# Performance work log

Measured on AMD Instinct MI355X. Metric: run time of the kernel, lower is better.

Reference implementation:

```python
import jax, jax.numpy as jnp
import numpy as np

N_NODES = 20000
N_EDGES = 640000
F_IN = 128
HID = 128


def setup_inputs() -> dict:
    key = jax.random.key(0)
    ks = jax.random.split(key, 12)
    d = {}
    d["x"] = jax.random.normal(ks[0], (N_NODES, F_IN), dtype=jnp.float32)
    d["edge_index"] = jax.random.randint(ks[1], (2, N_EDGES), 0, N_NODES, dtype=jnp.int64)
    d["edge_weight"] = jax.random.uniform(ks[2], (N_EDGES,), dtype=jnp.float32)
    d["h"] = jax.random.normal(ks[3], (N_NODES, HID), dtype=jnp.float32)
    s1 = 1.0 / np.sqrt(F_IN)
    s2 = 1.0 / np.sqrt(HID)
    s3 = 1.0 / np.sqrt(2 * HID)
    d["W1"] = jax.random.uniform(ks[4], (F_IN, HID), jnp.float32, -s1, s1)
    d["b1"] = jnp.zeros((HID,), jnp.float32)
    d["W2"] = jax.random.uniform(ks[5], (HID, HID), jnp.float32, -s2, s2)
    d["b2"] = jnp.zeros((HID,), jnp.float32)
    d["Wu"] = jax.random.uniform(ks[6], (2 * HID, HID), jnp.float32, -s3, s3)
    d["bu"] = jax.random.uniform(ks[7], (HID,), jnp.float32, -s3, s3)
    d["Wr"] = jax.random.uniform(ks[8], (2 * HID, HID), jnp.float32, -s3, s3)
    d["br"] = jax.random.uniform(ks[9], (HID,), jnp.float32, -s3, s3)
    d["Wc"] = jax.random.uniform(ks[10], (2 * HID, HID), jnp.float32, -s3, s3)
    d["bc"] = jax.random.uniform(ks[11], (HID,), jnp.float32, -s3, s3)
    return d


def _gcn_layer(x, W, b, src, dst, norm, n):
    # GCNConv: transform then normalized scatter-add aggregation
    xw = x @ W                                    # [N, out]
    agg = jax.ops.segment_sum(xw[src] * norm[:, None], dst, num_segments=n)
    return agg + b


def reference(x, edge_index, edge_weight, h, W1, b1, W2, b2, Wu, bu, Wr, br, Wc, bc):
    n = x.shape[0]
    loops = jnp.arange(n, dtype=edge_index.dtype)
    src = jnp.concatenate([edge_index[0], loops])
    dst = jnp.concatenate([edge_index[1], loops])
    ew = jnp.concatenate([edge_weight, jnp.ones((n,), edge_weight.dtype)])
    # symmetric GCN normalization with self-loops
    deg = jax.ops.segment_sum(ew, dst, num_segments=n)
    dinv = jnp.where(deg > 0, jax.lax.rsqrt(deg), 0.0)
    norm = dinv[src] * ew * dinv[dst]             # [E+N]
    # 2-layer GCN: in->hid (ReLU) -> hid->hid
    h1 = jax.nn.relu(_gcn_layer(x, W1, b1, src, dst, norm, n))
    g = _gcn_layer(h1, W2, b2, src, dst, norm, n)
    xg = jax.nn.sigmoid(g)                        # [N, HID]
    # GRU-style gating
    xh = jnp.concatenate([xg, h], axis=-1)        # [N, 2*HID]
    u = jax.nn.sigmoid(xh @ Wu + bu)
    r = jax.nn.sigmoid(xh @ Wr + br)
    c = jnp.tanh(jnp.concatenate([xg, r * h], axis=-1) @ Wc + bc)
    return u * h + (1.0 - u) * c
```

## Files before the change

### kernel.cpp

```cpp
#include <hip/hip_runtime.h>
#include <math.h>

#define N_NODES 20000
#define N_EDGES 640000
#define HID 128
#define NPAD 20224
#define NBLK 79

typedef __attribute__((ext_vector_type(8))) short bf16x8;
typedef __attribute__((ext_vector_type(4))) float f32x4;

#define FIX_SCALE 274877906944.0
#define FIX_MASK ((1ull << 48) - 1)

__device__ inline short f2bf(float f) {
    unsigned u = __builtin_bit_cast(unsigned, f);
    u += 0x7fffu + ((u >> 16) & 1u);
    return (short)(u >> 16);
}
__device__ inline float bf2f(short s) {
    unsigned u = ((unsigned)(unsigned short)s) << 16;
    return __builtin_bit_cast(float, u);
}
__device__ inline float4 unpack_bf4(uint2 v) {
    float4 f;
    f.x = __builtin_bit_cast(float, v.x << 16);
    f.y = __builtin_bit_cast(float, v.x & 0xffff0000u);
    f.z = __builtin_bit_cast(float, v.y << 16);
    f.w = __builtin_bit_cast(float, v.y & 0xffff0000u);
    return f;
}
__device__ inline uint2 pack_bf4(float4 f) {
    uint2 v;
    v.x = (unsigned)(unsigned short)f2bf(f.x) | ((unsigned)(unsigned short)f2bf(f.y) << 16);
    v.y = (unsigned)(unsigned short)f2bf(f.z) | ((unsigned)(unsigned short)f2bf(f.w) << 16);
    return v;
}

__global__ __launch_bounds__(256) void k_init(unsigned long long* packed) {
    int i = blockIdx.x * 256 + threadIdx.x;
    if (i < 4 * NPAD) packed[i] = 0ull;
}

__global__ __launch_bounds__(256) void k_hist(unsigned long long* packed, int* __restrict__ rank,
                                              const int* __restrict__ dst,
                                              const float* __restrict__ ew) {
    int e = blockIdx.x * 256 + threadIdx.x;
    int shard = blockIdx.x & 3;
    if (e < N_EDGES) {
        int d = dst[e];
        unsigned long long add = (1ull << 48) | (unsigned long long)((double)ew[e] * FIX_SCALE);
        unsigned long long old = atomicAdd(&packed[shard * NPAD + d], add);
        rank[e] = (int)(old >> 48);
    }
}

__global__ __launch_bounds__(256) void k_scan_part(const unsigned long long* __restrict__ packed,
                                                   int* __restrict__ tot, int* __restrict__ bsum) {
    __shared__ int red[256];
    int tid = threadIdx.x;
    int i = blockIdx.x * 256 + tid;
    int t = 0;
    if (i < N_NODES) {
#pragma unroll
        for (int s = 0; s < 4; s++) t += (int)(packed[s * NPAD + i] >> 48);
        tot[i] = t;
    }
    red[tid] = t;
    __syncthreads();
    for (int off = 128; off > 0; off >>= 1) {
        if (tid < off) red[tid] += red[tid + off];
        __syncthreads();
    }
    if (tid == 0) bsum[blockIdx.x] = red[0];
}

__global__ __launch_bounds__(128) void k_scan_bsum(const int* __restrict__ bsum,
                                                   int* __restrict__ boff) {
    __shared__ int smem[128];
    int tid = threadIdx.x;
    int v = (tid < NBLK) ? bsum[tid] : 0;
    smem[tid] = v;
    __syncthreads();
    for (int off = 1; off < 128; off <<= 1) {
        int t = (tid >= off) ? smem[tid - off] : 0;
        __syncthreads();
        smem[tid] += t;
        __syncthreads();
    }
    if (tid < NBLK) boff[tid] = smem[tid] - v;
}

__global__ __launch_bounds__(256) void k_scan_final(const unsigned long long* __restrict__ packed,
                                                    const int* __restrict__ tot,
                                                    const int* __restrict__ boff,
                                                    int* __restrict__ rp, int* __restrict__ sb,
                                                    float* __restrict__ dinv) {
    __shared__ int smem[256];
    int tid = threadIdx.x;
    int i = blockIdx.x * 256 + tid;
    int t = (i < N_NODES) ? tot[i] : 0;
    smem[tid] = t;
    __syncthreads();
    for (int off = 1; off < 256; off <<= 1) {
        int x = (tid >= off) ? smem[tid - off] : 0;
        __syncthreads();
        smem[tid] += x;
        __syncthreads();
    }
    if (i < N_NODES) {
        int excl = smem[tid] - t + boff[blockIdx.x];
        rp[i] = excl;
        if (i == N_NODES - 1) rp[N_NODES] = excl + t;
        int acc = excl;
        double deg = 1.0;
#pragma unroll
        for (int s = 0; s < 4; s++) {
            unsigned long long p = packed[s * NPAD + i];
            sb[s * NPAD + i] = acc;
            acc += (int)(p >> 48);
            deg += (double)(p & FIX_MASK) * (1.0 / FIX_SCALE);
        }
        dinv[i] = rsqrtf((float)deg);
    }
}

__global__ __launch_bounds__(256) void k_fill(const int* __restrict__ src,
                                              const int* __restrict__ dst,
                                              const float* __restrict__ ew,
                                              const float* __restrict__ dinv,
                                              const int* __restrict__ sb,
                                              const int* __restrict__ rank,
                                              int2* __restrict__ csr) {
    int e = blockIdx.x * 256 + threadIdx.x;
    int shard = blockIdx.x & 3;
    if (e < N_EDGES) {
        int s = src[e], d = dst[e];
        int slot = sb[shard * NPAD + d] + rank[e];
        float w = dinv[s] * ew[e] * dinv[d];
        csr[slot] = make_int2(s, __builtin_bit_cast(int, w));
    }
}

__global__ __launch_bounds__(256) void k_cvt2(const float* __restrict__ x, const float* __restrict__ h,
                                              short* __restrict__ xb, short* __restrict__ hb) {
    const int NH4 = (N_NODES * HID) / 4;
    int i = blockIdx.x * 256 + threadIdx.x;
    const float* s; short* d; int idx;
    if (i < NH4) { s = x; d = xb; idx = i; } else { s = h; d = hb; idx = i - NH4; }
    float4 v = ((const float4*)s)[idx];
    short4 o;
    o.x = f2bf(v.x); o.y = f2bf(v.y); o.z = f2bf(v.z); o.w = f2bf(v.w);
    ((short4*)d)[idx] = o;
}

__global__ __launch_bounds__(256) void k_wcvt(const float* __restrict__ W1, const float* __restrict__ W2,
                                              const float* __restrict__ Wu, const float* __restrict__ Wr,
                                              const float* __restrict__ Wc,
                                              short* WT1, short* WT2, short* WTu, short* WTr, short* WTc) {
    int i = blockIdx.x * 256 + threadIdx.x;
    if (i < 32768) {
        const float* W = (i < 16384) ? W1 : W2;
        short* T = (i < 16384) ? WT1 : WT2;
        int j = i & 16383;
        int n = j >> 7, k = j & 127;
        T[n * 128 + k] = f2bf(W[k * 128 + n]);
    } else {
        int j = i - 32768;
        const float* W = Wu; short* T = WTu;
        if (j >= 65536)      { W = Wc; T = WTc; j -= 65536; }
        else if (j >= 32768) { W = Wr; T = WTr; j -= 32768; }
        int n = j >> 8, k = j & 255;
        T[n * 256 + k] = f2bf(W[k * 128 + n]);
    }
}

__global__ __launch_bounds__(256) void k_gemm_mfma(const short* __restrict__ Ab,
                                                   const short* __restrict__ WT,
                                                   short* __restrict__ Cb) {
    __shared__ short As[16 * 136];
    int tid = threadIdx.x;
    int r0 = blockIdx.x * 16;
    {
        int row = tid >> 4;
        int col0 = (tid & 15) * 8;
        *(bf16x8*)(&As[row * 136 + col0]) = *(const bf16x8*)(Ab + (size_t)(r0 + row) * HID + col0);
    }
    __syncthreads();
    int wave = tid >> 6, lane = tid & 63;
    int m = lane & 15, quad = lane >> 4;
    f32x4 acc[2];
    acc[0] = (f32x4){0.f, 0.f, 0.f, 0.f};
    acc[1] = acc[0];
#pragma unroll
    for (int ks = 0; ks < 4; ks++) {
        int k0 = ks * 32 + quad * 8;
        bf16x8 a = *(const bf16x8*)(&As[m * 136 + k0]);
#pragma unroll
        for (int j = 0; j < 2; j++) {
            int n = (wave * 2 + j) * 16 + m;
            bf16x8 b = *(const bf16x8*)(WT + n * 128 + k0);
            acc[j] = __builtin_amdgcn_mfma_f32_16x16x32_bf16(a, b, acc[j], 0, 0, 0);
        }
    }
#pragma unroll
    for (int j = 0; j < 2; j++) {
        int col = (wave * 2 + j) * 16 + m;
#pragma unroll
        for (int rg = 0; rg < 4; rg++) {
            int grow = r0 + quad * 4 + rg;
            Cb[(size_t)grow * HID + col] = f2bf(acc[j][rg]);
        }
    }
}

__global__ __launch_bounds__(256) void k_aggregate(const short* __restrict__ xw,
                                                   short* __restrict__ outb,
                                                   const int* __restrict__ rp,
                                                   const int2* __restrict__ csr,
                                                   const float* __restrict__ dinv,
                                                   const float* __restrict__ bias,
                                                   int act) {
    int node = blockIdx.x * 4 + (threadIdx.x >> 6);
    int lane = threadIdx.x & 63;
    int half = lane >> 5;
    int l = lane & 31;
    float4 acc = {0.f, 0.f, 0.f, 0.f};
    if (half == 0) {
        float dv = dinv[node];
        float dv2 = dv * dv;
        float4 v = unpack_bf4(((const uint2*)(xw + (size_t)node * HID))[l]);
        acc.x = v.x * dv2; acc.y = v.y * dv2; acc.z = v.z * dv2; acc.w = v.w * dv2;
    }
    int j = rp[node], end = rp[node + 1];
    for (; j + 7 < end; j += 8) {
        int2 e0 = csr[j + 0 + half];
        int2 e1 = csr[j + 2 + half];
        int2 e2 = csr[j + 4 + half];
        int2 e3 = csr[j + 6 + half];
        float4 v0 = unpack_bf4(((const uint2*)(xw + (size_t)e0.x * HID))[l]);
        float4 v1 = unpack_bf4(((const uint2*)(xw + (size_t)e1.x * HID))[l]);
        float4 v2 = unpack_bf4(((const uint2*)(xw + (size_t)e2.x * HID))[l]);
        float4 v3 = unpack_bf4(((const uint2*)(xw + (size_t)e3.x * HID))[l]);
        float w0 = __builtin_bit_cast(float, e0.y);
        float w1 = __builtin_bit_cast(float, e1.y);
        float w2 = __builtin_bit_cast(float, e2.y);
        float w3 = __builtin_bit_cast(float, e3.y);
        acc.x += v0.x * w0; acc.y += v0.y * w0; acc.z += v0.z * w0; acc.w += v0.w * w0;
        acc.x += v1.x * w1; acc.y += v1.y * w1; acc.z += v1.z * w1; acc.w += v1.w * w1;
        acc.x += v2.x * w2; acc.y += v2.y * w2; acc.z += v2.z * w2; acc.w += v2.w * w2;
        acc.x += v3.x * w3; acc.y += v3.y * w3; acc.z += v3.z * w3; acc.w += v3.w * w3;
    }
    for (; j + 1 < end; j += 2) {
        int2 e0 = csr[j + half];
        float4 v0 = unpack_bf4(((const uint2*)(xw + (size_t)e0.x * HID))[l]);
        float w0 = __builtin_bit_cast(float, e0.y);
        acc.x += v0.x * w0; acc.y += v0.y * w0; acc.z += v0.z * w0; acc.w += v0.w * w0;
    }
    if (j < end && half == 0) {
        int2 e0 = csr[j];
        float4 v0 = unpack_bf4(((const uint2*)(xw + (size_t)e0.x * HID))[l]);
        float w0 = __builtin_bit_cast(float, e0.y);
        acc.x += v0.x * w0; acc.y += v0.y * w0; acc.z += v0.z * w0; acc.w += v0.w * w0;
    }
    acc.x += __shfl_xor(acc.x, 32);
    acc.y += __shfl_xor(acc.y, 32);
    acc.z += __shfl_xor(acc.z, 32);
    acc.w += __shfl_xor(acc.w, 32);
    if (half == 0) {
        float4 b = ((const float4*)bias)[l];
        acc.x += b.x; acc.y += b.y; acc.z += b.z; acc.w += b.w;
        if (act == 0) {
            acc.x = fmaxf(acc.x, 0.f); acc.y = fmaxf(acc.y, 0.f);
            acc.z = fmaxf(acc.z, 0.f); acc.w = fmaxf(acc.w, 0.f);
        } else {
            acc.x = 1.f / (1.f + __expf(-acc.x)); acc.y = 1.f / (1.f + __expf(-acc.y));
            acc.z = 1.f / (1.f + __expf(-acc.z)); acc.w = 1.f / (1.f + __expf(-acc.w));
        }
        ((uint2*)(outb + (size_t)node * HID))[l] = pack_bf4(acc);
    }
}

__global__ __launch_bounds__(256) void k_gate(const short* __restrict__ xgb, const short* __restrict__ hb,
                                              const float* __restrict__ hf,
                                              const short* __restrict__ WTu, const short* __restrict__ WTr,
                                              const short* __restrict__ WTc,
                                              const float* __restrict__ pbu, const float* __restrict__ pbr,
                                              const float* __restrict__ pbc,
                                              float* __restrict__ out) {
    __shared__ short Xs[16 * 264];
    int tid = threadIdx.x;
    int r0 = blockIdx.x * 16;
#pragma unroll
    for (int i = 0; i < 2; i++) {
        int c = tid + i * 256;
        int row = c >> 5;
        int col0 = (c & 31) * 8;
        int grow = r0 + row;
        bf16x8 v;
        if (col0 < 128) v = *(const bf16x8*)(xgb + (size_t)grow * HID + col0);
        else            v = *(const bf16x8*)(hb + (size_t)grow * HID + (col0 - 128));
        *(bf16x8*)(&Xs[row * 264 + col0]) = v;
    }
    __syncthreads();
    int wave = tid >> 6, lane = tid & 63;
    int m = lane & 15, quad = lane >> 4;
    f32x4 au[2], ar[2];
    au[0] = (f32x4){0.f, 0.f, 0.f, 0.f};
    au[1] = au[0]; ar[0] = au[0]; ar[1] = au[0];
#pragma unroll
    for (int ks = 0; ks < 8; ks++) {
        int k0 = ks * 32 + quad * 8;
        bf16x8 a = *(const bf16x8*)(&Xs[m * 264 + k0]);
#pragma unroll
        for (int j = 0; j < 2; j++) {
            int n = (wave * 2 + j) * 16 + m;
            bf16x8 bu_f = *(const bf16x8*)(WTu + n * 256 + k0);
            au[j] = __builtin_amdgcn_mfma_f32_16x16x32_bf16(a, bu_f, au[j], 0, 0, 0);
            bf16x8 br_f = *(const bf16x8*)(WTr + n * 256 + k0);
            ar[j] = __builtin_amdgcn_mfma_f32_16x16x32_bf16(a, br_f, ar[j], 0, 0, 0);
        }
    }
    __syncthreads();
#pragma unroll
    for (int j = 0; j < 2; j++) {
        int col = (wave * 2 + j) * 16 + m;
        float brv = pbr[col];
#pragma unroll
        for (int rg = 0; rg < 4; rg++) {
            int trow = quad * 4 + rg;
            float rv = 1.f / (1.f + __expf(-(ar[j][rg] + brv)));
            float hv = bf2f(Xs[trow * 264 + 128 + col]);
            Xs[trow * 264 + 128 + col] = f2bf(rv * hv);
        }
    }
    __syncthreads();
    f32x4 ac[2];
    ac[0] = (f32x4){0.f, 0.f, 0.f, 0.f};
    ac[1] = ac[0];
#pragma unroll
    for (int ks = 0; ks < 8; ks++) {
        int k0 = ks * 32 + quad * 8;
        bf16x8 a = *(const bf16x8*)(&Xs[m * 264 + k0]);
#pragma unroll
        for (int j = 0; j < 2; j++) {
            int n = (wave * 2 + j) * 16 + m;
            bf16x8 bc_f = *(const bf16x8*)(WTc + n * 256 + k0);
            ac[j] = __builtin_amdgcn_mfma_f32_16x16x32_bf16(a, bc_f, ac[j], 0, 0, 0);
        }
    }
#pragma unroll
    for (int j = 0; j < 2; j++) {
        int col = (wave * 2 + j) * 16 + m;
        float buv = pbu[col], bcv = pbc[col];
#pragma unroll
        for (int rg = 0; rg < 4; rg++) {
            int grow = r0 + quad * 4 + rg;
            float uv = 1.f / (1.f + __expf(-(au[j][rg] + buv)));
            float cv = tanhf(ac[j][rg] + bcv);
            float hv = hf[(size_t)grow * HID + col];
            out[(size_t)grow * HID + col] = uv * hv + (1.f - uv) * cv;
        }
    }
}

extern "C" void kernel_launch(void* const* d_in, const int* in_sizes, int n_in,
                              void* d_out, int out_size, void* d_ws, size_t ws_size,
                              hipStream_t stream) {
    const float* x  = (const float*)d_in[0];
    const int*   ei = (const int*)d_in[1];
    const float* ew = (const float*)d_in[2];
    const float* h  = (const float*)d_in[3];
    const float* W1 = (const float*)d_in[4];
    const float* b1 = (const float*)d_in[5];
    const float* W2 = (const float*)d_in[6];
    const float* b2 = (const float*)d_in[7];
    const float* Wu = (const float*)d_in[8];
    const float* bu = (const float*)d_in[9];
    const float* Wr = (const float*)d_in[10];
    const float* br = (const float*)d_in[11];
    const float* Wc = (const float*)d_in[12];
    const float* bc = (const float*)d_in[13];
    const int* src = ei;
    const int* dst = ei + N_EDGES;
    float* out = (float*)d_out;

    const size_t NH = (size_t)N_NODES * HID;
    float* ws = (float*)d_ws;
    float* dinv = ws;
    int*   rp   = (int*)(ws + NPAD);
    unsigned long long* packed = (unsigned long long*)(ws + 2 * NPAD);
    int*   sb   = (int*)(ws + 10 * NPAD);
    int*   tot  = (int*)(ws + 14 * NPAD);
    int*   bsum = (int*)(ws + 15 * NPAD);
    int*   boff = (int*)(ws + 15 * NPAD + 128);
    int*   rank = (int*)(ws + 15 * NPAD + 256);
    int2*  csr  = (int2*)(ws + 15 * NPAD + 256 + N_EDGES);
    short* xb  = (short*)(ws + 15 * NPAD + 256 + 3 * N_EDGES);
    short* hb  = xb + NH;
    short* xw  = hb + NH;
    short* h1b = xw + NH;
    short* xgb = h1b + NH;
    short* WT1 = xgb + NH;
    short* WT2 = WT1 + 16384;
    short* WTu = WT2 + 16384;
    short* WTr = WTu + 32768;
    short* WTc = WTr + 32768;

    k_init<<<(4 * NPAD + 255) / 256, 256, 0, stream>>>(packed);
    k_hist<<<N_EDGES / 256, 256, 0, stream>>>(packed, rank, dst, ew);
    k_scan_part<<<NBLK, 256, 0, stream>>>(packed, tot, bsum);
    k_scan_bsum<<<1, 128, 0, stream>>>(bsum, boff);
    k_scan_final<<<NBLK, 256, 0, stream>>>(packed, tot, boff, rp, sb, dinv);
    k_fill<<<N_EDGES / 256, 256, 0, stream>>>(src, dst, ew, dinv, sb, rank, csr);

    k_cvt2<<<(int)(2 * NH / 1024), 256, 0, stream>>>(x, h, xb, hb);
    k_wcvt<<<512, 256, 0, stream>>>(W1, W2, Wu, Wr, Wc, WT1, WT2, WTu, WTr, WTc);

    k_gemm_mfma<<<N_NODES / 16, 256, 0, stream>>>(xb, WT1, xw);
    k_aggregate<<<N_NODES / 4, 256, 0, stream>>>(xw, h1b, rp, csr, dinv, b1, 0);
    k_gemm_mfma<<<N_NODES / 16, 256, 0, stream>>>(h1b, WT2, xw);
    k_aggregate<<<N_NODES / 4, 256, 0, stream>>>(xw, xgb, rp, csr, dinv, b2, 1);
    k_gate<<<N_NODES / 16, 256, 0, stream>>>(xgb, hb, h, WTu, WTr, WTc, bu, br, bc, out);
}
```

Measured before the change: 257.8 us.

## Fuse bf16 conversion into GEMMs, merge scan kernels, widen atomic shards and aggregate unroll

Removes the separate fp32-to-bf16 conversion kernel by converting x inside the first GEMM's tile load and h inside the gate kernel's load. Folds the block-offset scan into k_scan_final, where each block reduces the preceding block sums itself, dropping one launch. Doubles the number of atomic histogram shards to cut contention, and adds a 16-edge unrolled loop in aggregation for more memory-level parallelism. In exchange there are more shard reads in the scan and higher register pressure in the aggregate loop.

```diff
diff --git a/kernel.cpp b/kernel.cpp
--- a/kernel.cpp
+++ b/kernel.cpp
@@ -6,6 +6,7 @@
 #define HID 128
 #define NPAD 20224
 #define NBLK 79
+#define NSHARD 8
 
 typedef __attribute__((ext_vector_type(8))) short bf16x8;
 typedef __attribute__((ext_vector_type(4))) float f32x4;
@@ -36,17 +37,23 @@
     v.y = (unsigned)(unsigned short)f2bf(f.z) | ((unsigned)(unsigned short)f2bf(f.w) << 16);
     return v;
 }
+__device__ inline bf16x8 cvt8(float4 a0, float4 a1) {
+    bf16x8 v;
+    v[0] = f2bf(a0.x); v[1] = f2bf(a0.y); v[2] = f2bf(a0.z); v[3] = f2bf(a0.w);
+    v[4] = f2bf(a1.x); v[5] = f2bf(a1.y); v[6] = f2bf(a1.z); v[7] = f2bf(a1.w);
+    return v;
+}
 
 __global__ __launch_bounds__(256) void k_init(unsigned long long* packed) {
     int i = blockIdx.x * 256 + threadIdx.x;
-    if (i < 4 * NPAD) packed[i] = 0ull;
+    if (i < NSHARD * NPAD) packed[i] = 0ull;
 }
 
 __global__ __launch_bounds__(256) void k_hist(unsigned long long* packed, int* __restrict__ rank,
                                               const int* __restrict__ dst,
                                               const float* __restrict__ ew) {
     int e = blockIdx.x * 256 + threadIdx.x;
-    int shard = blockIdx.x & 3;
+    int shard = blockIdx.x & (NSHARD - 1);
     if (e < N_EDGES) {
         int d = dst[e];
         unsigned long long add = (1ull << 48) | (unsigned long long)((double)ew[e] * FIX_SCALE);
@@ -63,7 +70,7 @@
     int t = 0;
     if (i < N_NODES) {
 #pragma unroll
-        for (int s = 0; s < 4; s++) t += (int)(packed[s * NPAD + i] >> 48);
+        for (int s = 0; s < NSHARD; s++) t += (int)(packed[s * NPAD + i] >> 48);
         tot[i] = t;
     }
     red[tid] = t;
@@ -75,33 +82,23 @@
     if (tid == 0) bsum[blockIdx.x] = red[0];
 }
 
-__global__ __launch_bounds__(128) void k_scan_bsum(const int* __restrict__ bsum,
-                                                   int* __restrict__ boff) {
-    __shared__ int smem[128];
-    int tid = threadIdx.x;
-    int v = (tid < NBLK) ? bsum[tid] : 0;
-    smem[tid] = v;
-    __syncthreads();
-    for (int off = 1; off < 128; off <<= 1) {
-        int t = (tid >= off) ? smem[tid - off] : 0;
-        __syncthreads();
-        smem[tid] += t;
-        __syncthreads();
-    }
-    if (tid < NBLK) boff[tid] = smem[tid] - v;
-}
-
 __global__ __launch_bounds__(256) void k_scan_final(const unsigned long long* __restrict__ packed,
                                                     const int* __restrict__ tot,
-                                                    const int* __restrict__ boff,
+                                                    const int* __restrict__ bsum,
                                                     int* __restrict__ rp, int* __restrict__ sb,
                                                     float* __restrict__ dinv) {
     __shared__ int smem[256];
+    __shared__ int red[256];
     int tid = threadIdx.x;
+    red[tid] = (tid < blockIdx.x) ? bsum[tid] : 0;
     int i = blockIdx.x * 256 + tid;
     int t = (i < N_NODES) ? tot[i] : 0;
     smem[tid] = t;
     __syncthreads();
+    for (int off = 128; off > 0; off >>= 1) {
+        if (tid < off) red[tid] += red[tid + off];
+        __syncthreads();
+    }
     for (int off = 1; off < 256; off <<= 1) {
         int x = (tid >= off) ? smem[tid - off] : 0;
         __syncthreads();
@@ -109,13 +106,13 @@
         __syncthreads();
     }
     if (i < N_NODES) {
-        int excl = smem[tid] - t + boff[blockIdx.x];
+        int excl = smem[tid] - t + red[0];
         rp[i] = excl;
         if (i == N_NODES - 1) rp[N_NODES] = excl + t;
         int acc = excl;
         double deg = 1.0;
 #pragma unroll
-        for (int s = 0; s < 4; s++) {
+        for (int s = 0; s < NSHARD; s++) {
             unsigned long long p = packed[s * NPAD + i];
             sb[s * NPAD + i] = acc;
             acc += (int)(p >> 48);
@@ -133,25 +130,13 @@
                                               const int* __restrict__ rank,
                                               int2* __restrict__ csr) {
     int e = blockIdx.x * 256 + threadIdx.x;
-    int shard = blockIdx.x & 3;
+    int shard = blockIdx.x & (NSHARD - 1);
     if (e < N_EDGES) {
         int s = src[e], d = dst[e];
         int slot = sb[shard * NPAD + d] + rank[e];
         float w = dinv[s] * ew[e] * dinv[d];
         csr[slot] = make_int2(s, __builtin_bit_cast(int, w));
     }
-}
-
-__global__ __launch_bounds__(256) void k_cvt2(const float* __restrict__ x, const float* __restrict__ h,
-                                              short* __restrict__ xb, short* __restrict__ hb) {
-    const int NH4 = (N_NODES * HID) / 4;
-    int i = blockIdx.x * 256 + threadIdx.x;
-    const float* s; short* d; int idx;
-    if (i < NH4) { s = x; d = xb; idx = i; } else { s = h; d = hb; idx = i - NH4; }
-    float4 v = ((const float4*)s)[idx];
-    short4 o;
-    o.x = f2bf(v.x); o.y = f2bf(v.y); o.z = f2bf(v.z); o.w = f2bf(v.w);
-    ((short4*)d)[idx] = o;
 }
 
 __global__ __launch_bounds__(256) void k_wcvt(const float* __restrict__ W1, const float* __restrict__ W2,
@@ -175,7 +160,8 @@
     }
 }
 
-__global__ __launch_bounds__(256) void k_gemm_mfma(const short* __restrict__ Ab,
+__global__ __launch_bounds__(256) void k_gemm_mfma(const float* __restrict__ Af,
+                                                   const short* __restrict__ Ab,
                                                    const short* __restrict__ WT,
                                                    short* __restrict__ Cb) {
     __shared__ short As[16 * 136];
@@ -184,7 +170,14 @@
     {
         int row = tid >> 4;
         int col0 = (tid & 15) * 8;
-        *(bf16x8*)(&As[row * 136 + col0]) = *(const bf16x8*)(Ab + (size_t)(r0 + row) * HID + col0);
+        bf16x8 v;
+        if (Af) {
+            const float* p = Af + (size_t)(r0 + row) * HID + col0;
+            v = cvt8(*(const float4*)p, *(const float4*)(p + 4));
+        } else {
+            v = *(const bf16x8*)(Ab + (size_t)(r0 + row) * HID + col0);
+        }
+        *(bf16x8*)(&As[row * 136 + col0]) = v;
     }
     __syncthreads();
     int wave = tid >> 6, lane = tid & 63;
@@ -233,23 +226,31 @@
         acc.x = v.x * dv2; acc.y = v.y * dv2; acc.z = v.z * dv2; acc.w = v.w * dv2;
     }
     int j = rp[node], end = rp[node + 1];
+    for (; j + 15 < end; j += 16) {
+        int2 e[8];
+#pragma unroll
+        for (int i = 0; i < 8; i++) e[i] = csr[j + 2 * i + half];
+        float4 v[8];
+#pragma unroll
+        for (int i = 0; i < 8; i++) v[i] = unpack_bf4(((const uint2*)(xw + (size_t)e[i].x * HID))[l]);
+#pragma unroll
+        for (int i = 0; i < 8; i++) {
+            float w = __builtin_bit_cast(float, e[i].y);
+            acc.x += v[i].x * w; acc.y += v[i].y * w; acc.z += v[i].z * w; acc.w += v[i].w * w;
+        }
+    }
     for (; j + 7 < end; j += 8) {
-        int2 e0 = csr[j + 0 + half];
-        int2 e1 = csr[j + 2 + half];
-        int2 e2 = csr[j + 4 + half];
-        int2 e3 = csr[j + 6 + half];
-        float4 v0 = unpack_bf4(((const uint2*)(xw + (size_t)e0.x * HID))[l]);
-        float4 v1 = unpack_bf4(((const uint2*)(xw + (size_t)e1.x * HID))[l]);
-        float4 v2 = unpack_bf4(((const uint2*)(xw + (size_t)e2.x * HID))[l]);
-        float4 v3 = unpack_bf4(((const uint2*)(xw + (size_t)e3.x * HID))[l]);
-        float w0 = __builtin_bit_cast(float, e0.y);
-        float w1 = __builtin_bit_cast(float, e1.y);
-        float w2 = __builtin_bit_cast(float, e2.y);
-        float w3 = __builtin_bit_cast(float, e3.y);
-        acc.x += v0.x * w0; acc.y += v0.y * w0; acc.z += v0.z * w0; acc.w += v0.w * w0;
-        acc.x += v1.x * w1; acc.y += v1.y * w1; acc.z += v1.z * w1; acc.w += v1.w * w1;
-        acc.x += v2.x * w2; acc.y += v2.y * w2; acc.z += v2.z * w2; acc.w += v2.w * w2;
-        acc.x += v3.x * w3; acc.y += v3.y * w3; acc.z += v3.z * w3; acc.w += v3.w * w3;
+        int2 e[4];
+#pragma unroll
+        for (int i = 0; i < 4; i++) e[i] = csr[j + 2 * i + half];
+        float4 v[4];
+#pragma unroll
+        for (int i = 0; i < 4; i++) v[i] = unpack_bf4(((const uint2*)(xw + (size_t)e[i].x * HID))[l]);
+#pragma unroll
+        for (int i = 0; i < 4; i++) {
+            float w = __builtin_bit_cast(float, e[i].y);
+            acc.x += v[i].x * w; acc.y += v[i].y * w; acc.z += v[i].z * w; acc.w += v[i].w * w;
+        }
     }
     for (; j + 1 < end; j += 2) {
         int2 e0 = csr[j + half];
@@ -281,7 +282,7 @@
     }
 }
 
-__global__ __launch_bounds__(256) void k_gate(const short* __restrict__ xgb, const short* __restrict__ hb,
+__global__ __launch_bounds__(256) void k_gate(const short* __restrict__ xgb,
                                               const float* __restrict__ hf,
                                               const short* __restrict__ WTu, const short* __restrict__ WTr,
                                               const short* __restrict__ WTc,
@@ -298,8 +299,12 @@
         int col0 = (c & 31) * 8;
         int grow = r0 + row;
         bf16x8 v;
-        if (col0 < 128) v = *(const bf16x8*)(xgb + (size_t)grow * HID + col0);
-        else            v = *(const bf16x8*)(hb + (size_t)grow * HID + (col0 - 128));
+        if (col0 < 128) {
+            v = *(const bf16x8*)(xgb + (size_t)grow * HID + col0);
+        } else {
+            const float* p = hf + (size_t)grow * HID + (col0 - 128);
+            v = cvt8(*(const float4*)p, *(const float4*)(p + 4));
+        }
         *(bf16x8*)(&Xs[row * 264 + col0]) = v;
     }
     __syncthreads();
@@ -390,15 +395,12 @@
     float* dinv = ws;
     int*   rp   = (int*)(ws + NPAD);
     unsigned long long* packed = (unsigned long long*)(ws + 2 * NPAD);
-    int*   sb   = (int*)(ws + 10 * NPAD);
-    int*   tot  = (int*)(ws + 14 * NPAD);
-    int*   bsum = (int*)(ws + 15 * NPAD);
-    int*   boff = (int*)(ws + 15 * NPAD + 128);
-    int*   rank = (int*)(ws + 15 * NPAD + 256);
-    int2*  csr  = (int2*)(ws + 15 * NPAD + 256 + N_EDGES);
-    short* xb  = (short*)(ws + 15 * NPAD + 256 + 3 * N_EDGES);
-    short* hb  = xb + NH;
-    short* xw  = hb + NH;
+    int*   sb   = (int*)(ws + 18 * NPAD);
+    int*   tot  = (int*)(ws + 26 * NPAD);
+    int*   bsum = (int*)(ws + 27 * NPAD);
+    int*   rank = (int*)(ws + 27 * NPAD + 128);
+    int2*  csr  = (int2*)(ws + 27 * NPAD + 128 + N_EDGES);
+    short* xw  = (short*)(ws + 27 * NPAD + 128 + 3 * N_EDGES);
     short* h1b = xw + NH;
     short* xgb = h1b + NH;
     short* WT1 = xgb + NH;
@@ -407,19 +409,17 @@
     short* WTr = WTu + 32768;
     short* WTc = WTr + 32768;
 
-    k_init<<<(4 * NPAD + 255) / 256, 256, 0, stream>>>(packed);
+    k_init<<<(NSHARD * NPAD + 255) / 256, 256, 0, stream>>>(packed);
     k_hist<<<N_EDGES / 256, 256, 0, stream>>>(packed, rank, dst, ew);
     k_scan_part<<<NBLK, 256, 0, stream>>>(packed, tot, bsum);
-    k_scan_bsum<<<1, 128, 0, stream>>>(bsum, boff);
-    k_scan_final<<<NBLK, 256, 0, stream>>>(packed, tot, boff, rp, sb, dinv);
+    k_scan_final<<<NBLK, 256, 0, stream>>>(packed, tot, bsum, rp, sb, dinv);
     k_fill<<<N_EDGES / 256, 256, 0, stream>>>(src, dst, ew, dinv, sb, rank, csr);
 
-    k_cvt2<<<(int)(2 * NH / 1024), 256, 0, stream>>>(x, h, xb, hb);
     k_wcvt<<<512, 256, 0, stream>>>(W1, W2, Wu, Wr, Wc, WT1, WT2, WTu, WTr, WTc);
 
-    k_gemm_mfma<<<N_NODES / 16, 256, 0, stream>>>(xb, WT1, xw);
+    k_gemm_mfma<<<N_NODES / 16, 256, 0, stream>>>(x, nullptr, WT1, xw);
     k_aggregate<<<N_NODES / 4, 256, 0, stream>>>(xw, h1b, rp, csr, dinv, b1, 0);
-    k_gemm_mfma<<<N_NODES / 16, 256, 0, stream>>>(h1b, WT2, xw);
+    k_gemm_mfma<<<N_NODES / 16, 256, 0, stream>>>(nullptr, h1b, WT2, xw);
     k_aggregate<<<N_NODES / 4, 256, 0, stream>>>(xw, xgb, rp, csr, dinv, b2, 1);
-    k_gate<<<N_NODES / 16, 256, 0, stream>>>(xgb, hb, h, WTu, WTr, WTc, bu, br, bc, out);
-}
+    k_gate<<<N_NODES / 16, 256, 0, stream>>>(xgb, h, WTu, WTr, WTc, bu, br, bc, out);
+}
```

New measurement: 252.1 us. 1.02x faster.
